# Kernel tuning notes

Hardware: AMD Instinct MI355X
Metric: run time of the kernel (lower is better)

Reference implementation:

```python
import jax, jax.numpy as jnp
import numpy as np

N_LAYER = 6
EPS = 1e-5
THETA = 2.0 ** 16


def _ln(x):
    # LayerNorm without affine params, eps=1e-5 (torch default)
    m = x.mean(-1, keepdims=True)
    v = ((x - m) ** 2).mean(-1, keepdims=True)
    return (x - m) * jax.lax.rsqrt(v + EPS)


def _rope(phases, v):
    # rotate-half over interleaved pairs, phases are in cycles (mod 1 -> radians)
    v_rot = jnp.stack([-v[..., 1::2], v[..., ::2]], axis=-1).reshape(v.shape)
    ph = (phases % 1.0) * (2.0 * jnp.pi)
    return v * jnp.cos(ph) + v_rot * jnp.sin(ph)


def _forward(x, conv_w, conv_b, pos_embed, encoder, encoder_v, decoder, freqs, head_w, head_b):
    B, Cin, H, W = x.shape
    nh, D, N = encoder.shape
    P = conv_w.shape[-1]
    hp, wp = H // P, W // P
    T = hp * wp
    # patch embed: Conv2d(k=P, s=P) == unfold + matmul
    xp = x.reshape(B, Cin, hp, P, wp, P)
    tokens = jnp.einsum('bchpwq,dcpq->bhwd', xp, conv_w).reshape(B, T, D) + conv_b
    h = tokens + pos_embed  # (B, T, D); the unit head dim is handled by einsum broadcasting
    phases = jnp.arange(T, dtype=jnp.float32).reshape(1, 1, T, 1) * freqs  # (1,1,T,N)
    scale = 1.0 / jnp.sqrt(jnp.asarray(N, dtype=x.dtype))
    for _ in range(N_LAYER):  # weights are SHARED across layers, as in the module
        hn = _ln(h)  # (B, T, D)
        x_sparse = jax.nn.relu(jnp.einsum('btd,hdn->bhtn', hn, encoder))  # (B,nh,T,N)
        qr = _rope(phases, x_sparse)
        scores = jax.nn.softmax(jnp.einsum('bhtn,bhsn->bhts', qr, qr) * scale, axis=-1)
        yKV = _ln(jnp.einsum('bhts,bsd->bhtd', scores, hn))  # V = ln'd x, broadcast over heads
        y_sparse = jax.nn.relu(jnp.einsum('bhtd,hdn->bhtn', yKV, encoder_v))
        xy_sparse = x_sparse * y_sparse  # (B,nh,T,N)
        z = xy_sparse.transpose(0, 2, 1, 3).reshape(B, T, nh * N)  # (B,T,nh*N), head-major flatten
        yMLP = _ln(z @ decoder)  # (B,T,D)
        h = _ln(hn + yMLP)
    pooled = _ln(h.mean(axis=1))  # (B,D)
    return pooled @ head_w.T + head_b


def setup_inputs():
    key = jax.random.key(0)
    B, Cin, H, P = 64, 3, 224, 16
    D, nh, mult, ncls = 768, 12, 8, 1000
    N = mult * D // nh  # 512
    T = (H // P) ** 2  # 196
    ks = jax.random.split(key, 7)

    def xav(k, shape, fan_in, fan_out):
        a = (6.0 / (fan_in + fan_out)) ** 0.5
        return jax.random.uniform(k, shape, jnp.float32, -a, a)

    x = jax.random.normal(ks[0], (B, Cin, H, H), jnp.float32)
    conv_w = xav(ks[1], (D, Cin, P, P), Cin * P * P, D)
    conv_b = jnp.zeros((D,), jnp.float32)
    pos_embed = jax.random.normal(ks[2], (1, T, D), jnp.float32) * 0.02
    encoder = xav(ks[3], (nh, D, N), D, N)
    encoder_v = xav(ks[4], (nh, D, N), D, N)
    decoder = xav(ks[5], (nh * N, D), nh * N, D)
    i = jnp.arange(N, dtype=jnp.float32)
    freqs = ((1.0 / THETA) ** ((i // 2) * 2.0 / N)).reshape(1, 1, 1, N)  # paired RoPE freqs
    head_w = xav(ks[6], (ncls, D), D, ncls)
    head_b = jnp.zeros((ncls,), jnp.float32)
    return dict(x=x, conv_w=conv_w, conv_b=conv_b, pos_embed=pos_embed,
                encoder=encoder, encoder_v=encoder_v, decoder=decoder,
                freqs=freqs, head_w=head_w, head_b=head_b)


def reference(x, conv_w, conv_b, pos_embed, encoder, encoder_v, decoder, freqs, head_w, head_b):
    return _forward(x, conv_w, conv_b, pos_embed, encoder, encoder_v, decoder, freqs, head_w, head_b)
```

## Files before the change

### kernel.cpp

```cpp
#include <hip/hip_runtime.h>
#include <hip/hip_bf16.h>


typedef short bf16x8 __attribute__((ext_vector_type(8)));
typedef float f32x4 __attribute__((ext_vector_type(4)));
typedef unsigned short u16;

#define LN_EPS 1e-5f
#define SM_SCALE 0.044194173824159216f
#define TWO_PI 6.283185307179586f
#define MC 3136

typedef __attribute__((address_space(3))) unsigned char* as3p;
typedef const __attribute__((address_space(1))) unsigned char* as1p;

__device__ __forceinline__ void gload16(const u16* g, u16* l) {
    __builtin_amdgcn_global_load_lds((as1p)(const void*)g, (as3p)(void*)l, 16, 0, 0);
}

__device__ __forceinline__ u16 f2bf(float f) {
    __hip_bfloat16 h = __float2bfloat16(f);
    return *reinterpret_cast<u16*>(&h);
}
__device__ __forceinline__ float bf2f(u16 u) {
    return __uint_as_float(((unsigned)u) << 16);
}

__device__ __forceinline__ float block_reduce_sum(float v, float* sm) {
    #pragma unroll
    for (int o = 32; o; o >>= 1) v += __shfl_xor(v, o);
    if ((threadIdx.x & 63) == 0) sm[threadIdx.x >> 6] = v;
    __syncthreads();
    float r = sm[0] + sm[1] + sm[2] + sm[3];
    __syncthreads();
    return r;
}

__device__ __forceinline__ void gemm_core64(const u16* __restrict__ A, int lda,
                                            const u16* __restrict__ Bt, int ldb,
                                            int ksteps, f32x4 acc[4][4],
                                            u16* lds_a, u16* lds_b) {
    const int tid = threadIdx.x;
    const int lane = tid & 63;
    const int wave = tid >> 6;
    const int wr = (wave >> 1) * 64;
    const int wc = (wave & 1) * 64;
    const int lr = lane & 15;
    const int lg = lane >> 4;
    const int rx = lr & 7;
    const int srow = tid >> 3;
    const int gslot = (tid & 7) ^ (srow & 7);
    const u16* ga = A + (long)srow * lda + gslot * 8;
    const u16* gb = Bt + (long)srow * ldb + gslot * 8;
    u16* la = lds_a + tid * 8;
    u16* lb = lds_b + tid * 8;
    for (int k0 = 0; k0 < ksteps; ++k0) {
        __syncthreads();
        #pragma unroll
        for (int j = 0; j < 4; ++j) {
            gload16(ga + (long)(j * 32) * lda, la + j * 2048);
            gload16(gb + (long)(j * 32) * ldb, lb + j * 2048);
        }
        ga += 64; gb += 64;
        __syncthreads();
        bf16x8 af[2][4], bfr[2][4];
        #pragma unroll
        for (int kk = 0; kk < 2; ++kk) {
            const int ps = ((lg + kk * 4) ^ rx) * 8;
            #pragma unroll
            for (int m = 0; m < 4; m++)
                af[kk][m] = *(const bf16x8*)&lds_a[(wr + 16 * m + lr) * 64 + ps];
            #pragma unroll
            for (int n = 0; n < 4; n++)
                bfr[kk][n] = *(const bf16x8*)&lds_b[(wc + 16 * n + lr) * 64 + ps];
        }
        #pragma unroll
        for (int kk = 0; kk < 2; ++kk)
            #pragma unroll
            for (int m = 0; m < 4; m++)
                #pragma unroll
                for (int n = 0; n < 4; n++)
                    acc[m][n] = __builtin_amdgcn_mfma_f32_16x16x32_bf16(
                        af[kk][m], bfr[kk][n], acc[m][n], 0, 0, 0);
    }
}

#define GEMM64_PROLOGUE                                 \
    __shared__ alignas(16) u16 lds_ab[2 * 128 * 64];    \
    u16* lds_a = lds_ab;                                \
    u16* lds_b = lds_ab + 128 * 64;                     \
    f32x4 acc[4][4];                                    \
    _Pragma("unroll")                                   \
    for (int m = 0; m < 4; m++)                         \
        _Pragma("unroll")                               \
        for (int n = 0; n < 4; n++)                     \
            acc[m][n] = (f32x4){0.f, 0.f, 0.f, 0.f};

#define EPI_VARS                                        \
    const int lane = threadIdx.x & 63;                  \
    const int wave = threadIdx.x >> 6;                  \
    const int ewr = (wave >> 1) * 64 + (lane >> 4) * 4; \
    const int ewc = (wave & 1) * 64 + (lane & 15);

__device__ __forceinline__ void gemm_core(const u16* __restrict__ A, int lda,
                                          const u16* __restrict__ Bt, int ldb,
                                          int ksteps, f32x4 acc[4][4],
                                          u16* lds_a, u16* lds_b) {
    const int tid = threadIdx.x;
    const int lane = tid & 63;
    const int wave = tid >> 6;
    const int wr = (wave >> 1) * 64;
    const int wc = (wave & 1) * 64;
    const int lr = lane & 15;
    const int lk = (lane >> 4) * 8;
    const int srow = tid >> 2;
    const int scol = (tid & 3) * 8;
    const u16* ga = A + (long)srow * lda + scol;
    const u16* gb = Bt + (long)srow * ldb + scol;
    const long ha = (long)64 * lda;
    const long hb = (long)64 * ldb;
    u16* la = lds_a + tid * 8;
    u16* lb = lds_b + tid * 8;
    for (int k0 = 0; k0 < ksteps; ++k0) {
        __syncthreads();
        gload16(ga, la);
        gload16(ga + ha, la + 2048);
        gload16(gb, lb);
        gload16(gb + hb, lb + 2048);
        ga += 32; gb += 32;
        __syncthreads();
        bf16x8 af[4], bfr[4];
        #pragma unroll
        for (int m = 0; m < 4; m++)
            af[m] = *(const bf16x8*)&lds_a[(wr + 16 * m + lr) * 32 + lk];
        #pragma unroll
        for (int n = 0; n < 4; n++)
            bfr[n] = *(const bf16x8*)&lds_b[(wc + 16 * n + lr) * 32 + lk];
        #pragma unroll
        for (int m = 0; m < 4; m++)
            #pragma unroll
            for (int n = 0; n < 4; n++)
                acc[m][n] = __builtin_amdgcn_mfma_f32_16x16x32_bf16(af[m], bfr[n], acc[m][n], 0, 0, 0);
    }
}

__global__ __launch_bounds__(256) void k_pack_patches(const float* __restrict__ x,
                                                      u16* __restrict__ ap) {
    int idx = blockIdx.x * 256 + threadIdx.x;
    int r = idx / 768, k = idx - r * 768;
    int b = r / 196, t = r - b * 196;
    int hp = t / 14, wp = t - hp * 14;
    int c = k >> 8, rem = k & 255, p = rem >> 4, q = rem & 15;
    long src = ((long)(b * 3 + c) * 224 + hp * 16 + p) * 224 + wp * 16 + q;
    ap[idx] = f2bf(x[src]);
}

__global__ __launch_bounds__(256) void k_cast(const float* __restrict__ s,
                                              u16* __restrict__ d, int n) {
    int i = blockIdx.x * 256 + threadIdx.x;
    if (i < n) d[i] = f2bf(s[i]);
}

__global__ __launch_bounds__(256) void k_transpose_cast(const float* __restrict__ src,
                                                        u16* __restrict__ dst,
                                                        int R, int C) {
    __shared__ float tile[32][33];
    int c0 = blockIdx.x * 32, r0 = blockIdx.y * 32;
    long base = (long)blockIdx.z * R * C;
    int i = threadIdx.x >> 5, j = threadIdx.x & 31;
    #pragma unroll
    for (int p = 0; p < 4; p++) {
        int rr = i + p * 8;
        tile[rr][j] = src[base + (long)(r0 + rr) * C + c0 + j];
    }
    __syncthreads();
    #pragma unroll
    for (int p = 0; p < 4; p++) {
        int rr = i + p * 8;
        dst[base + (long)(c0 + rr) * R + r0 + j] = f2bf(tile[j][rr]);
    }
}

__global__ __launch_bounds__(256) void k_rope_tab(const float* __restrict__ freqs,
                                                  float* __restrict__ tc,
                                                  float* __restrict__ ts) {
    int idx = blockIdx.x * 256 + threadIdx.x;
    int t = idx >> 9, n = idx & 511;
    float ph = (float)t * freqs[n];
    ph = (ph - floorf(ph)) * TWO_PI;
    tc[idx] = cosf(ph);
    ts[idx] = sinf(ph);
}

__global__ __launch_bounds__(256) void k_colsum(const float* __restrict__ encv,
                                                float* __restrict__ cs) {
    int h = blockIdx.y, c = blockIdx.x * 256 + threadIdx.x;
    const float* base = encv + (long)h * 768 * 512 + c;
    float a = 0.f;
    for (int d = 0; d < 768; d++) a += base[(long)d * 512];
    cs[h * 512 + c] = a;
}

__global__ __launch_bounds__(256) void k_gemm_tokens(const u16* __restrict__ ap,
                                                     const u16* __restrict__ bw,
                                                     const float* __restrict__ cb,
                                                     const float* __restrict__ pe,
                                                     float* __restrict__ hout) {
    GEMM64_PROLOGUE
    int row0 = blockIdx.x * 128, col0 = blockIdx.y * 128;
    gemm_core64(ap + (long)row0 * 768, 768, bw + (long)col0 * 768, 768, 12, acc, lds_a, lds_b);
    EPI_VARS
    const int tid = threadIdx.x;
    float* TF = (float*)lds_ab;
    #pragma unroll
    for (int hf = 0; hf < 2; ++hf) {
        __syncthreads();
        if ((ewr >> 6) == hf) {
            #pragma unroll
            for (int m = 0; m < 4; m++)
                #pragma unroll
                for (int n = 0; n < 4; n++)
                    #pragma unroll
                    for (int i = 0; i < 4; i++) {
                        int row = row0 + ewr + 16 * m + i;
                        int col = col0 + ewc + 16 * n;
                        int t = row % 196;
                        TF[(ewr - hf * 64 + 16 * m + i) * 128 + ewc + 16 * n] =
                            acc[m][n][i] + cb[col] + pe[t * 768 + col];
                    }
        }
        __syncthreads();
        #pragma unroll
        for (int q = 0; q < 8; ++q) {
            int chunk = tid + q * 256;
            int r = chunk >> 5, c = chunk & 31;
            *(f32x4*)&hout[(long)(row0 + hf * 64 + r) * 768 + col0 + c * 4] =
                *(f32x4*)&TF[r * 128 + c * 4];
        }
    }
}

__global__ __launch_bounds__(256) void k_gemm_xs(const u16* __restrict__ hnb,
                                                 const u16* __restrict__ enct,
                                                 const float* __restrict__ tc,
                                                 const float* __restrict__ tsn,
                                                 u16* __restrict__ xs,
                                                 u16* __restrict__ qr) {
    GEMM64_PROLOGUE
    int p = blockIdx.x + 25 * blockIdx.y;
    int w = (p & 7) * 150 + (p >> 3);
    int row0 = (w % 25) * 128, col0 = (w / 25) * 128;
    int head = col0 >> 9, nn0 = col0 & 511;
    gemm_core64(hnb + (long)row0 * 768, 768,
                enct + ((long)head * 512 + nn0) * 768, 768, 12, acc, lds_a, lds_b);
    EPI_VARS
    const int tid = threadIdx.x;
    u16* TU = lds_ab;
    __syncthreads();
    #pragma unroll
    for (int m = 0; m < 4; m++)
        #pragma unroll
        for (int n = 0; n < 4; n++)
            #pragma unroll
            for (int i = 0; i < 4; i++)
                TU[(ewr + 16 * m + i) * 128 + ewc + 16 * n] =
                    f2bf(fmaxf(acc[m][n][i], 0.f));
    __syncthreads();
    #pragma unroll
    for (int q = 0; q < 8; ++q) {
        int chunk = tid + q * 256;
        int r = chunk >> 4, c = chunk & 15;
        int row = row0 + r;
        if (row < MC)
            *(bf16x8*)&xs[((long)head * MC + row) * 512 + nn0 + c * 8] =
                *(bf16x8*)&TU[r * 128 + c * 8];
    }
    __syncthreads();
    #pragma unroll
    for (int m = 0; m < 4; m++)
        #pragma unroll
        for (int n = 0; n < 4; n++)
            #pragma unroll
            for (int i = 0; i < 4; i++) {
                int row = row0 + ewr + 16 * m + i;
                float v = fmaxf(acc[m][n][i], 0.f);
                float pp = __shfl_xor(v, 1);
                if (row < MC) {
                    int t = row % 196;
                    int nn = nn0 + ewc + 16 * n;
                    float cs = tc[t * 512 + nn], sn = tsn[t * 512 + nn];
                    float rot = (nn & 1) ? pp : -pp;
                    TU[(ewr + 16 * m + i) * 128 + ewc + 16 * n] =
                        f2bf(v * cs + rot * sn);
                }
            }
    __syncthreads();
    #pragma unroll
    for (int q = 0; q < 8; ++q) {
        int chunk = tid + q * 256;
        int r = chunk >> 4, c = chunk & 15;
        int row = row0 + r;
        if (row < MC)
            *(bf16x8*)&qr[((long)head * MC + row) * 512 + nn0 + c * 8] =
                *(bf16x8*)&TU[r * 128 + c * 8];
    }
}

__global__ __launch_bounds__(256) void k_attn(const u16* __restrict__ qr,
                                              const u16* __restrict__ hnT,
                                              u16* __restrict__ ykv,
                                              float* __restrict__ stats) {
    __shared__ alignas(16) u16 lds_a[128 * 32];
    __shared__ alignas(16) u16 lds_b[128 * 32];
    __shared__ alignas(16) u16 Pl[128 * 232];
    __shared__ float part[2][128][2];
    const int tid = threadIdx.x, lane = tid & 63, wave = tid >> 6;
    const int wr = (wave >> 1) * 64, wc = (wave & 1) * 64;
    const int lr = lane & 15, lk = (lane >> 4) * 8;
    const int row0 = blockIdx.x * 128, bh = blockIdx.y;
    const int bL = bh & 15;
    const u16* qbase = qr + (long)bh * 196 * 512;

    f32x4 acc0[4][4], acc1[4][4];
    #pragma unroll
    for (int m = 0; m < 4; m++)
        #pragma unroll
        for (int n = 0; n < 4; n++) {
            acc0[m][n] = (f32x4){0.f, 0.f, 0.f, 0.f};
            acc1[m][n] = (f32x4){0.f, 0.f, 0.f, 0.f};
        }
    gemm_core(qbase + (long)row0 * 512, 512, qbase, 512, 16, acc0, lds_a, lds_b);
    gemm_core(qbase + (long)row0 * 512, 512, qbase + 128 * 512, 512, 16, acc1, lds_a, lds_b);

    const int rb = wr + (lane >> 4) * 4;
    #pragma unroll
    for (int m = 0; m < 4; m++)
        #pragma unroll
        for (int i = 0; i < 4; i++) {
            float mx = -1e30f;
            #pragma unroll
            for (int n = 0; n < 4; n++) {
                int c0 = wc + 16 * n + lr;
                if (c0 < 196) mx = fmaxf(mx, acc0[m][n][i]);
                if (c0 + 128 < 196) mx = fmaxf(mx, acc1[m][n][i]);
            }
            #pragma unroll
            for (int o = 1; o < 16; o <<= 1) mx = fmaxf(mx, __shfl_xor(mx, o));
            if (lr == 0) part[0][rb + 16 * m + i][wave & 1] = mx;
        }
    __syncthreads();
    #pragma unroll
    for (int m = 0; m < 4; m++)
        #pragma unroll
        for (int i = 0; i < 4; i++) {
            int row = rb + 16 * m + i;
            float rmx = fmaxf(part[0][row][0], part[0][row][1]);
            float s = 0.f;
            #pragma unroll
            for (int n = 0; n < 4; n++) {
                int c0 = wc + 16 * n + lr;
                float e0 = (c0 < 196) ? __expf((acc0[m][n][i] - rmx) * SM_SCALE) : 0.f;
                float e1 = (c0 + 128 < 196) ? __expf((acc1[m][n][i] - rmx) * SM_SCALE) : 0.f;
                acc0[m][n][i] = e0; acc1[m][n][i] = e1;
                s += e0 + e1;
            }
            #pragma unroll
            for (int o = 1; o < 16; o <<= 1) s += __shfl_xor(s, o);
            if (lr == 0) part[1][row][wave & 1] = s;
        }
    __syncthreads();
    #pragma unroll
    for (int m = 0; m < 4; m++)
        #pragma unroll
        for (int i = 0; i < 4; i++) {
            int row = rb + 16 * m + i;
            float inv = 1.f / (part[1][row][0] + part[1][row][1]);
            #pragma unroll
            for (int n = 0; n < 4; n++) {
                int c0 = wc + 16 * n + lr;
                Pl[row * 232 + c0] = f2bf(acc0[m][n][i] * inv);
                if (c0 + 128 < 224)
                    Pl[row * 232 + c0 + 128] = f2bf(acc1[m][n][i] * inv);
            }
        }
    __syncthreads();
    { float* pf = &part[0][0][0]; pf[tid] = 0.f; pf[tid + 256] = 0.f; }
    const int srow = tid >> 2, scol = (tid & 3) * 8;
    for (int cd = 0; cd < 6; ++cd) {
        const u16* Bt = hnT + ((long)bL * 768 + cd * 128) * 224;
        f32x4 acc[4][4];
        #pragma unroll
        for (int m = 0; m < 4; m++)
            #pragma unroll
            for (int n = 0; n < 4; n++) acc[m][n] = (f32x4){0.f, 0.f, 0.f, 0.f};
        for (int k0 = 0; k0 < 7; ++k0) {
            __syncthreads();
            gload16(Bt + (long)srow * 224 + k0 * 32 + scol, lds_b + tid * 8);
            gload16(Bt + (long)(srow + 64) * 224 + k0 * 32 + scol, lds_b + 2048 + tid * 8);
            __syncthreads();
            bf16x8 af[4], bfr[4];
            #pragma unroll
            for (int m = 0; m < 4; m++)
                af[m] = *(const bf16x8*)&Pl[(wr + 16 * m + lr) * 232 + k0 * 32 + lk];
            #pragma unroll
            for (int n = 0; n < 4; n++)
                bfr[n] = *(const bf16x8*)&lds_b[(wc + 16 * n + lr) * 32 + lk];
            #pragma unroll
            for (int m = 0; m < 4; m++)
                #pragma unroll
                for (int n = 0; n < 4; n++)
                    acc[m][n] = __builtin_amdgcn_mfma_f32_16x16x32_bf16(af[m], bfr[n], acc[m][n], 0, 0, 0);
        }
        #pragma unroll
        for (int m = 0; m < 4; m++)
            #pragma unroll
            for (int i = 0; i < 4; i++) {
                float s = acc[m][0][i] + acc[m][1][i] + acc[m][2][i] + acc[m][3][i];
                float q2 = acc[m][0][i] * acc[m][0][i] + acc[m][1][i] * acc[m][1][i] +
                           acc[m][2][i] * acc[m][2][i] + acc[m][3][i] * acc[m][3][i];
                #pragma unroll
                for (int o = 1; o < 16; o <<= 1) {
                    s += __shfl_xor(s, o);
                    q2 += __shfl_xor(q2, o);
                }
                if (lr == 0) {
                    part[0][rb + 16 * m + i][wave & 1] += s;
                    part[1][rb + 16 * m + i][wave & 1] += q2;
                }
            }
        EPI_VARS
        #pragma unroll
        for (int m = 0; m < 4; m++)
            #pragma unroll
            for (int n = 0; n < 4; n++)
                #pragma unroll
                for (int i = 0; i < 4; i++) {
                    int trow = row0 + ewr + 16 * m + i;
                    if (trow < 196)
                        ykv[((long)bh * 196 + trow) * 768 + cd * 128 + ewc + 16 * n] =
                            f2bf(acc[m][n][i]);
                }
    }
    __syncthreads();
    if (tid < 128) {
        int trow = row0 + tid;
        if (trow < 196) {
            float s = part[0][tid][0] + part[0][tid][1];
            float q2 = part[1][tid][0] + part[1][tid][1];
            float mu = s * (1.f / 768.f);
            float var = q2 * (1.f / 768.f) - mu * mu;
            float2 st;
            st.x = mu;
            st.y = rsqrtf(var + LN_EPS);
            *(float2*)&stats[((long)bh * 196 + trow) * 2] = st;
        }
    }
}

__global__ __launch_bounds__(256) void k_gemm_ys(const u16* __restrict__ ykv,
                                                 const u16* __restrict__ encvt,
                                                 const u16* __restrict__ xs,
                                                 const float* __restrict__ stats,
                                                 const float* __restrict__ colsum,
                                                 u16* __restrict__ z) {
    GEMM64_PROLOGUE
    int p = blockIdx.x + 25 * (blockIdx.y + 4 * blockIdx.z);
    int w = (p & 7) * 150 + (p >> 3);
    int rt = w % 25, rem = w / 25;
    int ct = rem & 3, h = rem >> 2;
    int row0 = rt * 128, col0 = ct * 128;
    gemm_core64(ykv + ((long)h * MC + row0) * 768, 768,
                encvt + ((long)h * 512 + col0) * 768, 768, 12, acc, lds_a, lds_b);
    EPI_VARS
    const int tid = threadIdx.x;
    u16* TU = lds_ab;
    __syncthreads();
    #pragma unroll
    for (int q = 0; q < 8; ++q) {
        int chunk = tid + q * 256;
        int r = chunk >> 4, c = chunk & 15;
        *(bf16x8*)&TU[r * 128 + c * 8] =
            *(const bf16x8*)&xs[((long)h * MC + row0 + r) * 512 + col0 + c * 8];
    }
    __syncthreads();
    #pragma unroll
    for (int m = 0; m < 4; m++)
        #pragma unroll
        for (int i = 0; i < 4; i++) {
            int rloc = ewr + 16 * m + i;
            int row = row0 + rloc;
            float mu = 0.f, rs = 0.f;
            if (row < MC) {
                float2 st = *(const float2*)&stats[((long)h * MC + row) * 2];
                mu = st.x; rs = st.y;
            }
            #pragma unroll
            for (int n = 0; n < 4; n++) {
                int cloc = ewc + 16 * n;
                float cs = colsum[h * 512 + col0 + cloc];
                float v = (acc[m][n][i] - mu * cs) * rs;
                v = fmaxf(v, 0.f) * bf2f(TU[rloc * 128 + cloc]);
                TU[rloc * 128 + cloc] = f2bf(v);
            }
        }
    __syncthreads();
    #pragma unroll
    for (int q = 0; q < 8; ++q) {
        int chunk = tid + q * 256;
        int r = chunk >> 4, c = chunk & 15;
        int row = row0 + r;
        if (row < MC)
            *(bf16x8*)&z[(long)row * 6144 + h * 512 + col0 + c * 8] =
                *(bf16x8*)&TU[r * 128 + c * 8];
    }
}

__global__ __launch_bounds__(256) void k_gemm_mlp(const u16* __restrict__ z,
                                                  const u16* __restrict__ dect,
                                                  float* __restrict__ rawK) {
    GEMM64_PROLOGUE
    int p = blockIdx.x + 25 * (blockIdx.y + 6 * blockIdx.z);
    int w = (p & 7) * 75 + (p >> 3);
    int row0 = (w % 25) * 128, col0 = ((w / 25) % 6) * 128, s = w / 150;
    gemm_core64(z + (long)row0 * 6144 + s * 1536, 6144,
                dect + (long)col0 * 6144 + s * 1536, 6144, 24, acc, lds_a, lds_b);
    EPI_VARS
    const int tid = threadIdx.x;
    float* TF = (float*)lds_ab;
    float* raw = rawK + (long)s * MC * 768;
    #pragma unroll
    for (int hf = 0; hf < 2; ++hf) {
        __syncthreads();
        if ((ewr >> 6) == hf) {
            #pragma unroll
            for (int m = 0; m < 4; m++)
                #pragma unroll
                for (int n = 0; n < 4; n++)
                    #pragma unroll
                    for (int i = 0; i < 4; i++)
                        TF[(ewr - hf * 64 + 16 * m + i) * 128 + ewc + 16 * n] =
                            acc[m][n][i];
        }
        __syncthreads();
        #pragma unroll
        for (int q = 0; q < 8; ++q) {
            int chunk = tid + q * 256;
            int r = chunk >> 5, c = chunk & 31;
            int row = row0 + hf * 64 + r;
            if (row < MC)
                *(f32x4*)&raw[(long)row * 768 + col0 + c * 4] =
                    *(f32x4*)&TF[r * 128 + c * 4];
        }
    }
}

__global__ __launch_bounds__(256) void k_ln1(const float* __restrict__ h,
                                             u16* __restrict__ hnb) {
    __shared__ float sm[4];
    int r = blockIdx.x, tid = threadIdx.x;
    const float* p = h + (long)r * 768;
    float x0 = p[tid], x1 = p[tid + 256], x2 = p[tid + 512];
    float mean = block_reduce_sum(x0 + x1 + x2, sm) * (1.f / 768.f);
    float d0 = x0 - mean, d1 = x1 - mean, d2 = x2 - mean;
    float var = block_reduce_sum(d0 * d0 + d1 * d1 + d2 * d2, sm) * (1.f / 768.f);
    float rs = rsqrtf(var + LN_EPS);
    long ro = (long)r * 768;
    hnb[ro + tid] = f2bf(d0 * rs);
    hnb[ro + tid + 256] = f2bf(d1 * rs);
    hnb[ro + tid + 512] = f2bf(d2 * rs);
}

__global__ __launch_bounds__(256) void k_hnT(const u16* __restrict__ hnb,
                                             u16* __restrict__ hnT) {
    __shared__ u16 tile[32][33];
    int t0 = blockIdx.x * 32, d0 = blockIdx.y * 32, b = blockIdx.z;
    int i = threadIdx.x >> 5, j = threadIdx.x & 31;
    #pragma unroll
    for (int p = 0; p < 4; p++) {
        int t = t0 + i + p * 8;
        tile[i + p * 8][j] = (t < 196) ? hnb[((long)b * 196 + t) * 768 + d0 + j] : (u16)0;
    }
    __syncthreads();
    #pragma unroll
    for (int p = 0; p < 4; p++) {
        int dd = i + p * 8;
        hnT[((long)b * 768 + d0 + dd) * 224 + t0 + j] = tile[j][dd];
    }
}

__global__ __launch_bounds__(256) void k_final_h(const float* __restrict__ rawK,
                                                 u16* __restrict__ hnb) {
    __shared__ float sm[4];
    const long PS = (long)MC * 768;
    int r = blockIdx.x, tid = threadIdx.x;
    const float* rp = rawK + (long)r * 768;
    u16* hp = hnb + (long)r * 768;
    float y0 = rp[tid] + rp[tid + PS] + rp[tid + 2 * PS] + rp[tid + 3 * PS];
    float y1 = rp[tid + 256] + rp[tid + 256 + PS] + rp[tid + 256 + 2 * PS] + rp[tid + 256 + 3 * PS];
    float y2 = rp[tid + 512] + rp[tid + 512 + PS] + rp[tid + 512 + 2 * PS] + rp[tid + 512 + 3 * PS];
    float h0 = bf2f(hp[tid]), h1 = bf2f(hp[tid + 256]), h2 = bf2f(hp[tid + 512]);
    float mean = block_reduce_sum(y0 + y1 + y2, sm) * (1.f / 768.f);
    float d0 = y0 - mean, d1 = y1 - mean, d2 = y2 - mean;
    float var = block_reduce_sum(d0 * d0 + d1 * d1 + d2 * d2, sm) * (1.f / 768.f);
    float rs = rsqrtf(var + LN_EPS);
    float s0 = h0 + d0 * rs;
    float s1 = h1 + d1 * rs;
    float s2 = h2 + d2 * rs;
    mean = block_reduce_sum(s0 + s1 + s2, sm) * (1.f / 768.f);
    d0 = s0 - mean; d1 = s1 - mean; d2 = s2 - mean;
    var = block_reduce_sum(d0 * d0 + d1 * d1 + d2 * d2, sm) * (1.f / 768.f);
    rs = rsqrtf(var + LN_EPS);
    hp[tid] = f2bf(d0 * rs);
    hp[tid + 256] = f2bf(d1 * rs);
    hp[tid + 512] = f2bf(d2 * rs);
}

__global__ __launch_bounds__(256) void k_pool1(const u16* __restrict__ hnb,
                                               float* __restrict__ part) {
    int g = blockIdx.x, b = blockIdx.y, tid = threadIdx.x;
    const u16* base = hnb + ((long)b * 196 + g * 14) * 768;
    float a0 = 0.f, a1 = 0.f, a2 = 0.f;
    for (int t = 0; t < 14; t++) {
        const u16* p = base + (long)t * 768;
        a0 += bf2f(p[tid]); a1 += bf2f(p[tid + 256]); a2 += bf2f(p[tid + 512]);
    }
    float* pp = part + ((long)b * 14 + g) * 768;
    pp[tid] = a0; pp[tid + 256] = a1; pp[tid + 512] = a2;
}

__global__ __launch_bounds__(256) void k_pool2(const float* __restrict__ part,
                                               float* __restrict__ pooled) {
    __shared__ float sm[4];
    int b = blockIdx.x, tid = threadIdx.x;
    const float* pp = part + (long)b * 14 * 768;
    float a0 = 0.f, a1 = 0.f, a2 = 0.f;
    for (int g = 0; g < 14; g++) {
        a0 += pp[g * 768 + tid]; a1 += pp[g * 768 + tid + 256]; a2 += pp[g * 768 + tid + 512];
    }
    a0 *= (1.f / 196.f); a1 *= (1.f / 196.f); a2 *= (1.f / 196.f);
    float mean = block_reduce_sum(a0 + a1 + a2, sm) * (1.f / 768.f);
    float d0 = a0 - mean, d1 = a1 - mean, d2 = a2 - mean;
    float var = block_reduce_sum(d0 * d0 + d1 * d1 + d2 * d2, sm) * (1.f / 768.f);
    float rs = rsqrtf(var + LN_EPS);
    pooled[(long)b * 768 + tid] = d0 * rs;
    pooled[(long)b * 768 + tid + 256] = d1 * rs;
    pooled[(long)b * 768 + tid + 512] = d2 * rs;
}

__global__ __launch_bounds__(256) void k_head(const float* __restrict__ pooled,
                                              const float* __restrict__ hw,
                                              const float* __restrict__ hb,
                                              float* __restrict__ out) {
    __shared__ float pr[768];
    int b = blockIdx.y, tid = threadIdx.x;
    pr[tid] = pooled[(long)b * 768 + tid];
    pr[tid + 256] = pooled[(long)b * 768 + tid + 256];
    pr[tid + 512] = pooled[(long)b * 768 + tid + 512];
    __syncthreads();
    int c = blockIdx.x * 4 + (tid >> 6);
    int lane = tid & 63;
    const float* wrow = hw + (long)c * 768;
    float acc = 0.f;
    #pragma unroll
    for (int k = 0; k < 768; k += 64) acc += pr[k + lane] * wrow[k + lane];
    #pragma unroll
    for (int o = 32; o; o >>= 1) acc += __shfl_xor(acc, o);
    if (lane == 0) out[(long)b * 1000 + c] = acc + hb[c];
}

extern "C" void kernel_launch(void* const* d_in, const int* in_sizes, int n_in,
                              void* d_out, int out_size, void* d_ws, size_t ws_size,
                              hipStream_t stream) {
    const float* x     = (const float*)d_in[0];
    const float* convw = (const float*)d_in[1];
    const float* convb = (const float*)d_in[2];
    const float* pe    = (const float*)d_in[3];
    const float* enc   = (const float*)d_in[4];
    const float* encv  = (const float*)d_in[5];
    const float* dec   = (const float*)d_in[6];
    const float* freqs = (const float*)d_in[7];
    const float* hw    = (const float*)d_in[8];
    const float* hbias = (const float*)d_in[9];
    float* out = (float*)d_out;

    char* W = (char*)d_ws;
    size_t off = 0;
    auto ALLOC = [&](size_t bytes) {
        size_t o = off;
        off += (bytes + 255) & ~(size_t)255;
        return o;
    };
    float* bh    = (float*)(W + ALLOC(38535168));
    u16*   bhnb  = (u16*)  (W + ALLOC(19267584 + 524288));
    u16*   bhnT  = (u16*)  (W + ALLOC(22020096));
    u16*   benc  = (u16*)  (W + ALLOC(9437184));
    u16*   bencv = (u16*)  (W + ALLOC(9437184));
    u16*   bdec  = (u16*)  (W + ALLOC(9437184));
    float* btc   = (float*)(W + ALLOC(401408));
    float* bts   = (float*)(W + ALLOC(401408));
    float* bpool = (float*)(W + ALLOC(196608));
    float* bpart = (float*)(W + ALLOC(2752512));
    float* bstats= (float*)(W + ALLOC(301056));
    float* bcs   = (float*)(W + ALLOC(24576));
    char*  R1    = (char*) (W + ALLOC(38535168 + 2097152));
    char*  R2    = (char*) (W + ALLOC(57802752 + 524288));
    char*  R3    = (char*) (W + ALLOC(38535168 + 524288));
    (void)ws_size; (void)in_sizes; (void)n_in; (void)out_size;

    u16*   bap  = (u16*)R2;
    u16*   bcw  = (u16*)R3;
    u16*   qr   = (u16*)R1;
    u16*   z    = (u16*)R1;
    u16*   ykv  = (u16*)R2;
    float* rawK = (float*)R2;
    u16*   xs   = (u16*)R3;

    k_pack_patches<<<37632, 256, 0, stream>>>(x, bap);
    k_cast<<<2304, 256, 0, stream>>>(convw, bcw, 768 * 768);
    k_gemm_tokens<<<dim3(98, 6), 256, 0, stream>>>(bap, bcw, convb, pe, bh);
    k_transpose_cast<<<dim3(16, 24, 12), 256, 0, stream>>>(enc, benc, 768, 512);
    k_transpose_cast<<<dim3(16, 24, 12), 256, 0, stream>>>(encv, bencv, 768, 512);
    k_transpose_cast<<<dim3(24, 192, 1), 256, 0, stream>>>(dec, bdec, 6144, 768);
    k_rope_tab<<<392, 256, 0, stream>>>(freqs, btc, bts);
    k_colsum<<<dim3(2, 12), 256, 0, stream>>>(encv, bcs);
    k_ln1<<<12544, 256, 0, stream>>>(bh, bhnb);

    for (int L = 0; L < 6; ++L) {
        k_hnT<<<dim3(7, 24, 64), 256, 0, stream>>>(bhnb, bhnT);
        for (int c = 0; c < 4; ++c) {
            long r0 = (long)c * MC;
            k_gemm_xs<<<dim3(25, 48), 256, 0, stream>>>(
                bhnb + r0 * 768, benc, btc, bts, xs, qr);
            k_attn<<<dim3(2, 192), 256, 0, stream>>>(
                qr, bhnT + (long)c * 16 * 768 * 224, ykv, bstats);
            k_gemm_ys<<<dim3(25, 4, 12), 256, 0, stream>>>(ykv, bencv, xs, bstats, bcs, z);
            k_gemm_mlp<<<dim3(25, 6, 4), 256, 0, stream>>>(z, bdec, rawK);
            k_final_h<<<MC, 256, 0, stream>>>(rawK, bhnb + r0 * 768);
        }
    }

    k_pool1<<<dim3(14, 64), 256, 0, stream>>>(bhnb, bpart);
    k_pool2<<<64, 256, 0, stream>>>(bpart, bpool);
    k_head<<<dim3(250, 64), 256, 0, stream>>>(bpool, hw, hbias, out);
}
```

Before: 6.880 ms.

## Fuse RoPE into xs store pass and remap attention blocks for XCD locality

```diff
diff --git a/kernel.cpp b/kernel.cpp
--- a/kernel.cpp
+++ b/kernel.cpp
@@ -275,34 +275,34 @@
             *(bf16x8*)&xs[((long)head * MC + row) * 512 + nn0 + c * 8] =
                 *(bf16x8*)&TU[r * 128 + c * 8];
     }
-    __syncthreads();
-    #pragma unroll
-    for (int m = 0; m < 4; m++)
-        #pragma unroll
-        for (int n = 0; n < 4; n++)
-            #pragma unroll
-            for (int i = 0; i < 4; i++) {
-                int row = row0 + ewr + 16 * m + i;
-                float v = fmaxf(acc[m][n][i], 0.f);
-                float pp = __shfl_xor(v, 1);
-                if (row < MC) {
-                    int t = row % 196;
-                    int nn = nn0 + ewc + 16 * n;
-                    float cs = tc[t * 512 + nn], sn = tsn[t * 512 + nn];
-                    float rot = (nn & 1) ? pp : -pp;
-                    TU[(ewr + 16 * m + i) * 128 + ewc + 16 * n] =
-                        f2bf(v * cs + rot * sn);
-                }
-            }
-    __syncthreads();
     #pragma unroll
     for (int q = 0; q < 8; ++q) {
         int chunk = tid + q * 256;
         int r = chunk >> 4, c = chunk & 15;
         int row = row0 + r;
-        if (row < MC)
-            *(bf16x8*)&qr[((long)head * MC + row) * 512 + nn0 + c * 8] =
-                *(bf16x8*)&TU[r * 128 + c * 8];
+        if (row < MC) {
+            int t = row % 196;
+            int nn = nn0 + c * 8;
+            bf16x8 v8 = *(bf16x8*)&TU[r * 128 + c * 8];
+            f32x4 cs0 = *(const f32x4*)&tc[t * 512 + nn];
+            f32x4 cs1 = *(const f32x4*)&tc[t * 512 + nn + 4];
+            f32x4 sn0 = *(const f32x4*)&tsn[t * 512 + nn];
+            f32x4 sn1 = *(const f32x4*)&tsn[t * 512 + nn + 4];
+            float v[8], qv[8];
+            #pragma unroll
+            for (int j = 0; j < 8; j++) v[j] = bf2f((u16)v8[j]);
+            #pragma unroll
+            for (int j = 0; j < 2; j++) {
+                qv[2 * j]     = v[2 * j] * cs0[2 * j]     - v[2 * j + 1] * sn0[2 * j];
+                qv[2 * j + 1] = v[2 * j + 1] * cs0[2 * j + 1] + v[2 * j] * sn0[2 * j + 1];
+                qv[4 + 2 * j]     = v[4 + 2 * j] * cs1[2 * j]     - v[4 + 2 * j + 1] * sn1[2 * j];
+                qv[4 + 2 * j + 1] = v[4 + 2 * j + 1] * cs1[2 * j + 1] + v[4 + 2 * j] * sn1[2 * j + 1];
+            }
+            bf16x8 o8;
+            #pragma unroll
+            for (int j = 0; j < 8; j++) o8[j] = (short)f2bf(qv[j]);
+            *(bf16x8*)&qr[((long)head * MC + row) * 512 + nn] = o8;
+        }
     }
 }
 
@@ -317,8 +317,13 @@
     const int tid = threadIdx.x, lane = tid & 63, wave = tid >> 6;
     const int wr = (wave >> 1) * 64, wc = (wave & 1) * 64;
     const int lr = lane & 15, lk = (lane >> 4) * 8;
-    const int row0 = blockIdx.x * 128, bh = blockIdx.y;
-    const int bL = bh & 15;
+    const int p = blockIdx.x;
+    const int xcd = p & 7, slot = p >> 3;
+    const int bL = 2 * xcd + (slot >= 24);
+    const int sub = (slot >= 24) ? slot - 24 : slot;
+    const int h = sub >> 1, rt = sub & 1;
+    const int bh = h * 16 + bL;
+    const int row0 = rt * 128;
     const u16* qbase = qr + (long)bh * 196 * 512;
 
     f32x4 acc0[4][4], acc1[4][4];
@@ -731,7 +736,7 @@
             long r0 = (long)c * MC;
             k_gemm_xs<<<dim3(25, 48), 256, 0, stream>>>(
                 bhnb + r0 * 768, benc, btc, bts, xs, qr);
-            k_attn<<<dim3(2, 192), 256, 0, stream>>>(
+            k_attn<<<384, 256, 0, stream>>>(
                 qr, bhnT + (long)c * 16 * 768 * 224, ykv, bstats);
             k_gemm_ys<<<dim3(25, 4, 12), 256, 0, stream>>>(ykv, bencv, xs, bstats, bcs, z);
             k_gemm_mlp<<<dim3(25, 6, 4), 256, 0, stream>>>(z, bdec, rawK);
```

Measured after the change: 6.049 ms. 1.14x faster.
